# Kernel optimization log

Measured on AMD Instinct MI355X. Metric: run time of the kernel, lower is better.

## Reference

```python
import jax, jax.numpy as jnp
import numpy as np

B, N, D, E = 4, 1024, 1024, 8
TOP_N = 2
THRESHOLD = 0.2
EPS = 1e-9
CAP_FACTOR = 2.0
MIN_EXPERT_CAPACITY = 4
H = int(D * 4 * 2 / 3)  # GEGLU hidden = 2730


def setup_inputs() -> dict:
    key = jax.random.key(0)
    ks = jax.random.split(key, 8)
    u = lambda k, shape, fan: jax.random.uniform(k, shape, jnp.float32, -1.0, 1.0) * (fan ** -0.5)
    return {
        "x": jax.random.normal(ks[0], (B, N, D), jnp.float32),
        "route_probs": jax.random.uniform(ks[1], (TOP_N, B, N), jnp.float32),
        "gate_w": u(ks[2], (D, E), D),
        "w1": u(ks[3], (E, D, 2 * H), 2 * H),
        "b1": u(ks[4], (E, 2 * H), 2 * H),
        "mult_bias": jnp.ones((E, H), jnp.float32),
        "w2": u(ks[5], (E, H, D), D),
        "b2": u(ks[6], (E, D), D),
    }


def reference(x, route_probs, gate_w, w1, b1, mult_bias, w2, b2):
    b, n, d = x.shape
    e = gate_w.shape[1]
    cap = max(min(n, int(n * CAP_FACTOR / e)), MIN_EXPERT_CAPACITY)  # 256

    # ---- top-n gating ----
    logits = jnp.einsum('bnd,de->bne', x, gate_w)
    raw_gates = jax.nn.softmax(logits, axis=-1)
    gate_vals, gate_idx = jax.lax.top_k(raw_gates, TOP_N)          # [b,n,k]
    gate_vals = jnp.moveaxis(gate_vals, -1, 0)                      # [k,b,n]
    gate_idx = jnp.moveaxis(gate_idx, -1, 0)                        # [k,b,n]
    one_hot_idx = jax.nn.one_hot(gate_idx, e, dtype=x.dtype)        # [k,b,n,e]

    denom = jnp.clip(gate_vals.sum(axis=0, keepdims=True), EPS)
    gate_vals = gate_vals / denom

    # route to expert k>0 with prob min(1, gate/threshold); expert 0 always routed
    should_route = route_probs < (gate_vals / THRESHOLD)
    should_route = should_route.at[0].set(True)
    mask = one_hot_idx * should_route[..., None].astype(x.dtype)    # [k,b,n,e]

    # exclusive cumsum over sequence dim -> position within each expert
    mask_cumsum = jnp.cumsum(mask, axis=2) - mask                   # [k,b,n,e]

    positions, masks = [], []
    prev_count = jnp.zeros((b, 1, e), x.dtype)
    for k in range(TOP_N):  # small fixed loop over top-n
        pos_e = (mask_cumsum[k] + prev_count) * mask[k]             # [b,n,e]
        mk = mask[k] * (pos_e < float(cap)).astype(x.dtype)
        prev_count = prev_count + mk.sum(axis=1, keepdims=True)
        positions.append(pos_e.sum(axis=-1))                        # [b,n]
        masks.append(mk)
    positions = jnp.stack(positions)                                # [k,b,n]
    mask = jnp.stack(masks)                                         # [k,b,n,e]

    mask_flat = mask.sum(axis=-1)                                   # [k,b,n] in {0,1}
    gates = gate_vals * mask_flat
    pos_one_hot = jax.nn.one_hot(positions.astype(jnp.int32), cap, dtype=x.dtype)  # [k,b,n,c]

    # combine tensor [b,n,e,c]; dispatch is its boolean support
    combine = jnp.einsum('kbn,kbne,kbnc->bnec', gates * mask_flat, one_hot_idx, pos_one_hot)
    dispatch = (combine > 0).astype(x.dtype)

    # ---- dispatch tokens to experts ----
    xe = jnp.einsum('bnd,bnec->ebcd', x, dispatch)                  # [e,b,c,d]

    # ---- per-expert GEGLU FFN (grouped GEMM) ----
    h = jnp.einsum('ebcd,edf->ebcf', xe, w1) + b1[:, None, None, :]
    val, gate = jnp.split(h, 2, axis=-1)
    act = jax.nn.gelu(gate, approximate=False) * val * mult_bias[:, None, None, :]
    out_e = jnp.einsum('ebch,ehd->ebcd', act, w2) + b2[:, None, None, :]

    # ---- combine ----
    out = jnp.einsum('ebcd,bnec->bnd', out_e, combine)
    return out


if __name__ == '__main__':
    inp = setup_inputs()
    o = reference(**inp)
    print(o.shape, o.dtype)
```

## Files before the change

kernel.cpp:

```cpp
#include <hip/hip_runtime.h>
#include <hip/hip_bf16.h>
#include <math.h>

#define B_ 4
#define N_ 1024
#define D_ 1024
#define E_ 8
#define H_ 2730
#define H2_ 5460
#define CAP_ 256
#define NTOK 4096
#define NSLOT 8192
#define NKT1 16
#define NKT2 43
#define NFG 22

typedef __attribute__((ext_vector_type(8))) short short8;
typedef __attribute__((ext_vector_type(4))) float f32x4;

__device__ __forceinline__ unsigned short f2bf(float f) {
    __hip_bfloat16 h = __float2bfloat16(f);
    return *reinterpret_cast<unsigned short*>(&h);
}

#define GLL16(g, l)                                                          \
    __builtin_amdgcn_global_load_lds(                                        \
        (const __attribute__((address_space(1))) void*)(g),                  \
        (__attribute__((address_space(3))) void*)(l), 16, 0, 0)

#define VMCNT4() asm volatile("s_waitcnt vmcnt(4)" ::: "memory")
#define VMCNT3() asm volatile("s_waitcnt vmcnt(3)" ::: "memory")
#define VMCNT0() asm volatile("s_waitcnt vmcnt(0)" ::: "memory")
#define SBAR()   __builtin_amdgcn_s_barrier()
#define SCHEDB() __builtin_amdgcn_sched_barrier(0)


__global__ __launch_bounds__(256) void k_cvt1(const float* __restrict__ w1,
                                              unsigned short* __restrict__ w1p) {
    const int fg = blockIdx.x;
    const int kt = blockIdx.y;
    const int e  = blockIdx.z;
    const float* w1e = w1 + (size_t)e * D_ * H2_;
    unsigned short* dst = w1p + (((size_t)((e * NFG + fg) * NKT1 + kt)) << 14);
#pragma unroll
    for (int i = 0; i < 8; ++i) {
        const int o = i * 256 + threadIdx.x;
        const int l = o & 63, n16 = (o >> 6) & 15, k32 = o >> 10;
        const int f = fg * 128 + ((n16 & 7) << 4) + (l & 15);
        const int k = kt * 64 + (k32 << 5) + ((l >> 4) << 3);
        ushort4 r0 = {0, 0, 0, 0}, r1 = {0, 0, 0, 0};
        if (f < H_) {
            const float* s = w1e + (size_t)k * H2_ + (n16 >= 8 ? H_ : 0) + f;
            r0.x = f2bf(s[0]);
            r0.y = f2bf(s[(size_t)H2_]);
            r0.z = f2bf(s[(size_t)2 * H2_]);
            r0.w = f2bf(s[(size_t)3 * H2_]);
            r1.x = f2bf(s[(size_t)4 * H2_]);
            r1.y = f2bf(s[(size_t)5 * H2_]);
            r1.z = f2bf(s[(size_t)6 * H2_]);
            r1.w = f2bf(s[(size_t)7 * H2_]);
        }
        *reinterpret_cast<ushort4*>(dst + (size_t)o * 8) = r0;
        *reinterpret_cast<ushort4*>(dst + (size_t)o * 8 + 4) = r1;
    }
}

__global__ __launch_bounds__(256) void k_cvt2(const float* __restrict__ w2,
                                              unsigned short* __restrict__ w2p) {
    const int kt = blockIdx.x;
    const int nt = blockIdx.y;
    const int e  = blockIdx.z;
    const float* w2e = w2 + (size_t)e * H_ * D_;
    unsigned short* dst = w2p + (((size_t)((e * 8 + nt) * NKT2 + kt)) << 13);
#pragma unroll
    for (int i = 0; i < 4; ++i) {
        const int o = i * 256 + threadIdx.x;
        const int l = o & 63, n16 = (o >> 6) & 7, k32 = o >> 9;
        const int d = nt * 128 + (n16 << 4) + (l & 15);
        const int f = kt * 64 + (k32 << 5) + ((l >> 4) << 3);
        const float* s = w2e + (size_t)f * D_ + d;
        ushort4 r0, r1;
        r0.x = (f + 0 < H_) ? f2bf(s[0]) : 0;
        r0.y = (f + 1 < H_) ? f2bf(s[(size_t)D_]) : 0;
        r0.z = (f + 2 < H_) ? f2bf(s[(size_t)2 * D_]) : 0;
        r0.w = (f + 3 < H_) ? f2bf(s[(size_t)3 * D_]) : 0;
        r1.x = (f + 4 < H_) ? f2bf(s[(size_t)4 * D_]) : 0;
        r1.y = (f + 5 < H_) ? f2bf(s[(size_t)5 * D_]) : 0;
        r1.z = (f + 6 < H_) ? f2bf(s[(size_t)6 * D_]) : 0;
        r1.w = (f + 7 < H_) ? f2bf(s[(size_t)7 * D_]) : 0;
        *reinterpret_cast<ushort4*>(dst + (size_t)o * 8) = r0;
        *reinterpret_cast<ushort4*>(dst + (size_t)o * 8 + 4) = r1;
    }
}

__global__ __launch_bounds__(256) void k_gate(const float* __restrict__ x,
                                              const float* __restrict__ route,
                                              const float* __restrict__ gw,
                                              int* __restrict__ tokE,
                                              float* __restrict__ tokG,
                                              int* __restrict__ tokR) {
    const int wave = threadIdx.x >> 6, lane = threadIdx.x & 63;
    const int t = blockIdx.x * 4 + wave;
    float acc[E_];
#pragma unroll
    for (int e = 0; e < E_; ++e) acc[e] = 0.f;
    const float* xr = x + (size_t)t * D_;
    for (int d = lane; d < D_; d += 64) {
        float xv = xr[d];
        const float* g = gw + d * E_;
#pragma unroll
        for (int e = 0; e < E_; ++e) acc[e] = fmaf(xv, g[e], acc[e]);
    }
#pragma unroll
    for (int e = 0; e < E_; ++e) {
#pragma unroll
        for (int off = 32; off; off >>= 1) acc[e] += __shfl_xor(acc[e], off);
    }
    if (lane == 0) {
        float m = acc[0];
#pragma unroll
        for (int e = 1; e < E_; ++e) m = fmaxf(m, acc[e]);
        float p[E_]; float s = 0.f;
#pragma unroll
        for (int e = 0; e < E_; ++e) { p[e] = expf(acc[e] - m); s += p[e]; }
        int i0 = 0; float v0 = p[0];
#pragma unroll
        for (int e = 1; e < E_; ++e) if (p[e] > v0) { v0 = p[e]; i0 = e; }
        int i1 = (i0 == 0) ? 1 : 0; float v1 = p[i1];
#pragma unroll
        for (int e = 0; e < E_; ++e) if (e != i0 && p[e] > v1) { v1 = p[e]; i1 = e; }
        float p0 = v0 / s, p1 = v1 / s;
        float denom = fmaxf(p0 + p1, 1e-9f);
        float g0 = p0 / denom, g1 = p1 / denom;
        int r1 = route[NTOK + t] < (g1 / 0.2f);
        tokE[t] = i0; tokE[NTOK + t] = i1;
        tokG[t] = g0; tokG[NTOK + t] = g1;
        tokR[t] = r1;
    }
}

__global__ __launch_bounds__(256) void k_pos(const int* __restrict__ tokE,
                                             const float* __restrict__ tokG,
                                             const int* __restrict__ tokR,
                                             int* __restrict__ sot,
                                             int* __restrict__ tos) {
    const int e = blockIdx.x & 7, b = blockIdx.x >> 3;
    const int t = threadIdx.x;
    __shared__ int sc[256];
    const int base_bt = b * N_ + t * 4;
    int m0[4], m1[4];
    int c0 = 0, c1 = 0;
#pragma unroll
    for (int i = 0; i < 4; ++i) {
        int bt = base_bt + i;
        m0[i] = (tokE[bt] == e) ? 1 : 0;
        m1[i] = ((tokE[NTOK + bt] == e) && tokR[bt]) ? 1 : 0;
        c0 += m0[i]; c1 += m1[i];
    }
    int packed = c0 | (c1 << 16);
    sc[t] = packed;
    __syncthreads();
    for (int off = 1; off < 256; off <<= 1) {
        int v = (t >= off) ? sc[t - off] : 0;
        __syncthreads();
        sc[t] += v;
        __syncthreads();
    }
    int incl = sc[t];
    int total = sc[255];
    int excl = incl - packed;
    int base0 = excl & 0xffff;
    int base1 = excl >> 16;
    int kept0 = min(total & 0xffff, CAP_);
#pragma unroll
    for (int i = 0; i < 4; ++i) {
        int bt = base_bt + i;
        if (m0[i]) {
            int pos = base0++;
            if (pos < CAP_ && tokG[bt] > 0.f) {
                int s = ((e * B_ + b) << 8) + pos;
                sot[bt] = s;
                tos[s] = bt;
            }
        }
        if (m1[i]) {
            int pos = (base1++) + kept0;
            if (pos < CAP_ && tokG[NTOK + bt] > 0.f) {
                int s = ((e * B_ + b) << 8) + pos;
                sot[NTOK + bt] = s;
                tos[s] = bt;
            }
        }
    }
}

__global__ __launch_bounds__(256) void k_disp(const float* __restrict__ x,
                                              const int* __restrict__ tos,
                                              unsigned short* __restrict__ xeP) {
    const int t = threadIdx.x;
    const int s = blockIdx.x * 2 + (t >> 7);
    const int q = t & 127;
    const int bt = tos[s];
    const int kt = q >> 3, k32 = (q >> 2) & 1, kq = q & 3;
    const int lane = (kq << 4) | (s & 15);
    const int m16 = (s >> 4) & 15;
    const int sgrp = s >> 8;
    unsigned short* dst = xeP + (((size_t)(sgrp * NKT1 + kt)) << 14) + (k32 << 13) + (m16 << 9) + lane * 8;
    ushort4 r0 = {0, 0, 0, 0}, r1 = {0, 0, 0, 0};
    if (bt >= 0) {
        const float4 v0 = *reinterpret_cast<const float4*>(x + ((size_t)bt << 10) + q * 8);
        const float4 v1 = *reinterpret_cast<const float4*>(x + ((size_t)bt << 10) + q * 8 + 4);
        r0.x = f2bf(v0.x); r0.y = f2bf(v0.y); r0.z = f2bf(v0.z); r0.w = f2bf(v0.w);
        r1.x = f2bf(v1.x); r1.y = f2bf(v1.y); r1.z = f2bf(v1.z); r1.w = f2bf(v1.w);
    }
    *reinterpret_cast<ushort4*>(dst) = r0;
    *reinterpret_cast<ushort4*>(dst + 4) = r1;
}

__global__ __launch_bounds__(512) void k_ffn1(const unsigned short* __restrict__ xeP,
                                              const unsigned short* __restrict__ w1p,
                                              const float* __restrict__ b1,
                                              const float* __restrict__ mbias,
                                              unsigned short* __restrict__ actP) {
    const int wg = blockIdx.x;
    const int e = wg & 7;
    const int rem = wg >> 3;
    const int fg = rem >> 2;
    const int rt = rem & 3;
    const int sgrp = e * 4 + rt;

    __shared__ unsigned short Ab[2][16384];
    __shared__ unsigned short Bb[2][16384];

    const int tid = threadIdx.x, lane = tid & 63, w = tid >> 6;
    const int wm = w >> 2, wn = w & 3;
    const int lane8 = lane * 8;
    const int woff = w * 1024;
    const int am0 = wm * 8, bn0 = wn * 2;

    const unsigned short* abase = xeP + ((size_t)(sgrp * NKT1) << 14);
    const unsigned short* bbase = w1p + ((size_t)((e * NFG + fg) * NKT1) << 14);

    f32x4 acc[8][4];
#pragma unroll
    for (int i = 0; i < 8; ++i)
#pragma unroll
        for (int j = 0; j < 4; ++j) acc[i][j] = (f32x4)(0.f);

#define LDA1(ks, m16) (*reinterpret_cast<const short8*>(&Ab[cur][(((ks) << 4) + (m16)) * 512 + lane8]))
#define LDB1(ks, n16) (*reinterpret_cast<const short8*>(&Bb[cur][(((ks) << 4) + (n16)) * 512 + lane8]))

    {
#pragma unroll
        for (int hq = 0; hq < 2; ++hq) {
            const int off = hq * 8192 + woff;
            GLL16(abase + off + lane8, (char*)&Ab[0][off]);
            GLL16(abase + off + 512 + lane8, (char*)&Ab[0][off + 512]);
            GLL16(bbase + off + lane8, (char*)&Bb[0][off]);
            GLL16(bbase + off + 512 + lane8, (char*)&Bb[0][off + 512]);
        }
    }

    for (int kt = 0; kt < NKT1; ++kt) {
        const int cur = kt & 1, nx = cur ^ 1;
        const bool pf = (kt + 1 < NKT1);
        const unsigned short* asn = abase + ((size_t)(kt + 1) << 14);
        const unsigned short* bsn = bbase + ((size_t)(kt + 1) << 14);
        short8 af[4], bf[4];

        SCHEDB(); VMCNT4(); SBAR(); SCHEDB();

        if (pf) {
            GLL16(asn + woff + lane8, (char*)&Ab[nx][woff]);
            GLL16(asn + woff + 512 + lane8, (char*)&Ab[nx][woff + 512]);
        }
        bf[0] = LDB1(0, bn0); bf[1] = LDB1(0, bn0 + 1);
        bf[2] = LDB1(0, bn0 + 8); bf[3] = LDB1(0, bn0 + 9);
        af[0] = LDA1(0, am0 + 0); af[1] = LDA1(0, am0 + 1);
        af[2] = LDA1(0, am0 + 2); af[3] = LDA1(0, am0 + 3);
        __builtin_amdgcn_s_setprio(1);
#pragma unroll
        for (int mi = 0; mi < 4; ++mi)
#pragma unroll
            for (int n = 0; n < 4; ++n)
                acc[mi][n] = __builtin_amdgcn_mfma_f32_16x16x32_bf16(af[mi], bf[n], acc[mi][n], 0, 0, 0);
        __builtin_amdgcn_s_setprio(0);

        if (pf) {
            GLL16(bsn + woff + lane8, (char*)&Bb[nx][woff]);
            GLL16(bsn + woff + 512 + lane8, (char*)&Bb[nx][woff + 512]);
        }
        af[0] = LDA1(0, am0 + 4); af[1] = LDA1(0, am0 + 5);
        af[2] = LDA1(0, am0 + 6); af[3] = LDA1(0, am0 + 7);
        __builtin_amdgcn_s_setprio(1);
#pragma unroll
        for (int mi = 0; mi < 4; ++mi)
#pragma unroll
            for (int n = 0; n < 4; ++n)
                acc[4 + mi][n] = __builtin_amdgcn_mfma_f32_16x16x32_bf16(af[mi], bf[n], acc[4 + mi][n], 0, 0, 0);
        __builtin_amdgcn_s_setprio(0);

        SCHEDB();
        if (pf) { VMCNT4(); } else { VMCNT0(); }
        SBAR(); SCHEDB();

        if (pf) {
            const int off = 8192 + woff;
            GLL16(asn + off + lane8, (char*)&Ab[nx][off]);
            GLL16(asn + off + 512 + lane8, (char*)&Ab[nx][off + 512]);
        }
        bf[0] = LDB1(1, bn0); bf[1] = LDB1(1, bn0 + 1);
        bf[2] = LDB1(1, bn0 + 8); bf[3] = LDB1(1, bn0 + 9);
        af[0] = LDA1(1, am0 + 0); af[1] = LDA1(1, am0 + 1);
        af[2] = LDA1(1, am0 + 2); af[3] = LDA1(1, am0 + 3);
        __builtin_amdgcn_s_setprio(1);
#pragma unroll
        for (int mi = 0; mi < 4; ++mi)
#pragma unroll
            for (int n = 0; n < 4; ++n)
                acc[mi][n] = __builtin_amdgcn_mfma_f32_16x16x32_bf16(af[mi], bf[n], acc[mi][n], 0, 0, 0);
        __builtin_amdgcn_s_setprio(0);

        if (pf) {
            const int off = 8192 + woff;
            GLL16(bsn + off + lane8, (char*)&Bb[nx][off]);
            GLL16(bsn + off + 512 + lane8, (char*)&Bb[nx][off + 512]);
        }
        af[0] = LDA1(1, am0 + 4); af[1] = LDA1(1, am0 + 5);
        af[2] = LDA1(1, am0 + 6); af[3] = LDA1(1, am0 + 7);
        __builtin_amdgcn_s_setprio(1);
#pragma unroll
        for (int mi = 0; mi < 4; ++mi)
#pragma unroll
            for (int n = 0; n < 4; ++n)
                acc[4 + mi][n] = __builtin_amdgcn_mfma_f32_16x16x32_bf16(af[mi], bf[n], acc[4 + mi][n], 0, 0, 0);
        __builtin_amdgcn_s_setprio(0);
    }
#undef LDA1
#undef LDB1

    const float* b1e = b1 + (size_t)e * H2_;
    const float* mbe = mbias + (size_t)e * H_;
    const int colL = lane & 15, rq4 = (lane >> 4) * 4;
#pragma unroll
    for (int mi = 0; mi < 8; ++mi) {
        const int Rl = wm * 128 + mi * 16 + rq4;
#pragma unroll
        for (int vi = 0; vi < 2; ++vi) {
            const int f = fg * 128 + wn * 32 + vi * 16 + colL;
            if (f >= NKT2 * 64) continue;
            const bool real = f < H_;
            const float bv = real ? b1e[f] : 0.f;
            const float bg = real ? b1e[H_ + f] : 0.f;
            const float mv = real ? mbe[f] : 0.f;
            const int ktf = f >> 6, k32f = (f >> 5) & 1;
            const int lhi = ((f >> 3) & 3) << 4;
            const int bb = f & 7;
            const size_t cbase = ((size_t)(sgrp * NKT2 + ktf) << 14) + (k32f << 13);
#pragma unroll
            for (int j = 0; j < 4; ++j) {
                const int R = Rl + j;
                float a = 0.f;
                if (real) {
                    const float val = acc[mi][vi][j] + bv;
                    const float gt  = acc[mi][2 + vi][j] + bg;
                    a = 0.5f * gt * (1.f + erff(gt * 0.70710678118654752f)) * val * mv;
                }
                actP[cbase + ((R >> 4) << 9) + (size_t)((lhi | (R & 15)) * 8 + bb)] = f2bf(a);
            }
        }
    }
}

__global__ __launch_bounds__(512) void k_ffn2(const unsigned short* __restrict__ actP,
                                              const unsigned short* __restrict__ w2p,
                                              const float* __restrict__ b2,
                                              float* __restrict__ oute) {
    const int wg = blockIdx.x;
    const int e = wg & 7;
    const int rem = wg >> 3;
    const int nt = rem >> 2;
    const int mt = rem & 3;
    const int sgrp = e * 4 + mt;

    __shared__ unsigned short Ab[2][16384];
    __shared__ unsigned short Bb[2][8192];

    const int tid = threadIdx.x, lane = tid & 63, w = tid >> 6;
    const int wm = w >> 2, wn = w & 3;
    const int lane8 = lane * 8;
    const int woff = w * 1024;
    const int woffb = w * 512;
    const int am0 = wm * 8, bn0 = wn * 2;

    const unsigned short* abase = actP + ((size_t)(sgrp * NKT2) << 14);
    const unsigned short* bbase = w2p + ((size_t)((e * 8 + nt) * NKT2) << 13);

    f32x4 acc[8][2];
#pragma unroll
    for (int i = 0; i < 8; ++i)
#pragma unroll
        for (int j = 0; j < 2; ++j) acc[i][j] = (f32x4)(0.f);

#define LDA2(ks, m16) (*reinterpret_cast<const short8*>(&Ab[cur][(((ks) << 4) + (m16)) * 512 + lane8]))
#define LDB2(ks, n16) (*reinterpret_cast<const short8*>(&Bb[cur][((ks) * 8 + (n16)) * 512 + lane8]))

    {
#pragma unroll
        for (int hq = 0; hq < 2; ++hq) {
            const int off = hq * 8192 + woff;
            GLL16(abase + off + lane8, (char*)&Ab[0][off]);
            GLL16(abase + off + 512 + lane8, (char*)&Ab[0][off + 512]);
            const int boff = hq * 4096 + woffb;
            GLL16(bbase + boff + lane8, (char*)&Bb[0][boff]);
        }
    }

    for (int kt = 0; kt < NKT2; ++kt) {
        const int cur = kt & 1, nx = cur ^ 1;
        const bool pf = (kt + 1 < NKT2);
        const unsigned short* asn = abase + ((size_t)(kt + 1) << 14);
        const unsigned short* bsn = bbase + ((size_t)(kt + 1) << 13);
        short8 af[4], bf[2];

        SCHEDB(); VMCNT3(); SBAR(); SCHEDB();

        if (pf) {
            GLL16(asn + woff + lane8, (char*)&Ab[nx][woff]);
            GLL16(asn + woff + 512 + lane8, (char*)&Ab[nx][woff + 512]);
        }
        bf[0] = LDB2(0, bn0); bf[1] = LDB2(0, bn0 + 1);
        af[0] = LDA2(0, am0 + 0); af[1] = LDA2(0, am0 + 1);
        af[2] = LDA2(0, am0 + 2); af[3] = LDA2(0, am0 + 3);
        __builtin_amdgcn_s_setprio(1);
#pragma unroll
        for (int mi = 0; mi < 4; ++mi)
#pragma unroll
            for (int n = 0; n < 2; ++n)
                acc[mi][n] = __builtin_amdgcn_mfma_f32_16x16x32_bf16(af[mi], bf[n], acc[mi][n], 0, 0, 0);
        __builtin_amdgcn_s_setprio(0);

        if (pf) {
            GLL16(bsn + woffb + lane8, (char*)&Bb[nx][woffb]);
        }
        af[0] = LDA2(0, am0 + 4); af[1] = LDA2(0, am0 + 5);
        af[2] = LDA2(0, am0 + 6); af[3] = LDA2(0, am0 + 7);
        __builtin_amdgcn_s_setprio(1);
#pragma unroll
        for (int mi = 0; mi < 4; ++mi)
#pragma unroll
            for (int n = 0; n < 2; ++n)
                acc[4 + mi][n] = __builtin_amdgcn_mfma_f32_16x16x32_bf16(af[mi], bf[n], acc[4 + mi][n], 0, 0, 0);
        __builtin_amdgcn_s_setprio(0);

        SCHEDB();
        if (pf) { VMCNT3(); } else { VMCNT0(); }
        SBAR(); SCHEDB();

        if (pf) {
            const int off = 8192 + woff;
            GLL16(asn + off + lane8, (char*)&Ab[nx][off]);
            GLL16(asn + off + 512 + lane8, (char*)&Ab[nx][off + 512]);
        }
        bf[0] = LDB2(1, bn0); bf[1] = LDB2(1, bn0 + 1);
        af[0] = LDA2(1, am0 + 0); af[1] = LDA2(1, am0 + 1);
        af[2] = LDA2(1, am0 + 2); af[3] = LDA2(1, am0 + 3);
        __builtin_amdgcn_s_setprio(1);
#pragma unroll
        for (int mi = 0; mi < 4; ++mi)
#pragma unroll
            for (int n = 0; n < 2; ++n)
                acc[mi][n] = __builtin_amdgcn_mfma_f32_16x16x32_bf16(af[mi], bf[n], acc[mi][n], 0, 0, 0);
        __builtin_amdgcn_s_setprio(0);

        if (pf) {
            const int boff = 4096 + woffb;
            GLL16(bsn + boff + lane8, (char*)&Bb[nx][boff]);
        }
        af[0] = LDA2(1, am0 + 4); af[1] = LDA2(1, am0 + 5);
        af[2] = LDA2(1, am0 + 6); af[3] = LDA2(1, am0 + 7);
        __builtin_amdgcn_s_setprio(1);
#pragma unroll
        for (int mi = 0; mi < 4; ++mi)
#pragma unroll
            for (int n = 0; n < 2; ++n)
                acc[4 + mi][n] = __builtin_amdgcn_mfma_f32_16x16x32_bf16(af[mi], bf[n], acc[4 + mi][n], 0, 0, 0);
        __builtin_amdgcn_s_setprio(0);
    }
#undef LDA2
#undef LDB2

    const float* b2e = b2 + (size_t)e * D_;
    const int colL = lane & 15, rq4 = (lane >> 4) * 4;
#pragma unroll
    for (int mi = 0; mi < 8; ++mi) {
#pragma unroll
        for (int vi = 0; vi < 2; ++vi) {
            const int d = nt * 128 + wn * 32 + vi * 16 + colL;
            const float bb2 = b2e[d];
#pragma unroll
            for (int j = 0; j < 4; ++j) {
                const int R = mt * 256 + wm * 128 + mi * 16 + rq4 + j;
                oute[((size_t)(e * 1024 + R) << 10) + d] = acc[mi][vi][j] + bb2;
            }
        }
    }
}

__global__ __launch_bounds__(256) void k_comb(const float* __restrict__ oute,
                                              const int* __restrict__ sot,
                                              const float* __restrict__ tokG,
                                              float* __restrict__ out) {
    const int bt = blockIdx.x;
    const int t = threadIdx.x;
    const int s0 = sot[bt], s1 = sot[NTOK + bt];
    const float g0 = tokG[bt], g1 = tokG[NTOK + bt];
    float r0 = 0.f, r1 = 0.f, r2 = 0.f, r3 = 0.f;
    if (s0 >= 0) {
        const float4 v = *reinterpret_cast<const float4*>(oute + ((size_t)s0 << 10) + t * 4);
        r0 += g0 * v.x; r1 += g0 * v.y; r2 += g0 * v.z; r3 += g0 * v.w;
    }
    if (s1 >= 0) {
        const float4 v = *reinterpret_cast<const float4*>(oute + ((size_t)s1 << 10) + t * 4);
        r0 += g1 * v.x; r1 += g1 * v.y; r2 += g1 * v.z; r3 += g1 * v.w;
    }
    float4 o; o.x = r0; o.y = r1; o.z = r2; o.w = r3;
    *reinterpret_cast<float4*>(out + ((size_t)bt << 10) + t * 4) = o;
}

extern "C" void kernel_launch(void* const* d_in, const int* in_sizes, int n_in,
                              void* d_out, int out_size, void* d_ws, size_t ws_size,
                              hipStream_t stream) {
    const float* x     = (const float*)d_in[0];
    const float* route = (const float*)d_in[1];
    const float* gw    = (const float*)d_in[2];
    const float* w1    = (const float*)d_in[3];
    const float* b1    = (const float*)d_in[4];
    const float* mb    = (const float*)d_in[5];
    const float* w2    = (const float*)d_in[6];
    const float* b2    = (const float*)d_in[7];
    float* out = (float*)d_out;

    char* ws = (char*)d_ws;
    int*   tokE = (int*)(ws + 0);
    float* tokG = (float*)(ws + 32768);
    int*   tokR = (int*)(ws + 65536);
    int*   sot  = (int*)(ws + 81920);
    int*   tos  = (int*)(ws + 114688);
    unsigned short* xeP  = (unsigned short*)(ws + 147456);
    unsigned short* actP = (unsigned short*)(ws + 16924672);
    unsigned short* w1p  = (unsigned short*)(ws + 62013440);
    unsigned short* w2p  = (unsigned short*)(ws + 62013440);
    float* oute = (float*)(ws + 107102208);

    hipMemsetAsync(sot, 0xFF, 65536, stream);

    k_cvt1<<<dim3(NFG, NKT1, 8), 256, 0, stream>>>(w1, w1p);
    k_gate<<<NTOK / 4, 256, 0, stream>>>(x, route, gw, tokE, tokG, tokR);
    k_pos<<<E_ * B_, 256, 0, stream>>>(tokE, tokG, tokR, sot, tos);
    k_disp<<<NSLOT / 2, 256, 0, stream>>>(x, tos, xeP);
    k_ffn1<<<704, 512, 0, stream>>>(xeP, w1p, b1, mb, actP);
    k_cvt2<<<dim3(NKT2, 8, 8), 256, 0, stream>>>(w2, w2p);
    k_ffn2<<<256, 512, 0, stream>>>(actP, w2p, b2, oute);
    k_comb<<<NTOK, 256, 0, stream>>>(oute, sot, tokG, out);
}
```

Measured before the change: 370.4 us.

## Unroll GEMM k-loops by two with static LDS buffers and store expert outputs as bf16

Both grouped GEMM kernels now unroll their k-tile loop by two and alternate between separately named LDS buffers. Buffer indices are compile-time constants, which removes runtime buffer indexing and may let the compiler schedule LDS reads and MFMAs more freely. Separately, the second FFN writes its per-expert outputs in bf16 instead of fp32, and the combine kernel reads and widens them, halving the intermediate write and read traffic. This costs some precision on the expert outputs before the gated combine.

```diff
diff --git a/kernel.cpp b/kernel.cpp
--- a/kernel.cpp
+++ b/kernel.cpp
@@ -22,6 +22,10 @@
     __hip_bfloat16 h = __float2bfloat16(f);
     return *reinterpret_cast<unsigned short*>(&h);
 }
+__device__ __forceinline__ float bf2f(unsigned short u) {
+    unsigned x = ((unsigned)u) << 16;
+    union { unsigned u; float f; } c; c.u = x; return c.f;
+}
 
 #define GLL16(g, l)                                                          \
     __builtin_amdgcn_global_load_lds(                                        \
@@ -33,6 +37,7 @@
 #define VMCNT0() asm volatile("s_waitcnt vmcnt(0)" ::: "memory")
 #define SBAR()   __builtin_amdgcn_s_barrier()
 #define SCHEDB() __builtin_amdgcn_sched_barrier(0)
+#define MFMA16(a, b, c) __builtin_amdgcn_mfma_f32_16x16x32_bf16((a), (b), (c), 0, 0, 0)
 
 
 __global__ __launch_bounds__(256) void k_cvt1(const float* __restrict__ w1,
@@ -217,6 +222,80 @@
     *reinterpret_cast<ushort4*>(dst + 4) = r1;
 }
 
+#define LDF(BUF, idx) (*reinterpret_cast<const short8*>(&BUF[(idx) * 512 + lane8]))
+
+#define FFN1_MM03(AF0, AF1, AF2, AF3)                                         \
+    do {                                                                      \
+        acc[0][0]=MFMA16(AF0,bf0,acc[0][0]); acc[0][1]=MFMA16(AF0,bf1,acc[0][1]); \
+        acc[0][2]=MFMA16(AF0,bf2,acc[0][2]); acc[0][3]=MFMA16(AF0,bf3,acc[0][3]); \
+        acc[1][0]=MFMA16(AF1,bf0,acc[1][0]); acc[1][1]=MFMA16(AF1,bf1,acc[1][1]); \
+        acc[1][2]=MFMA16(AF1,bf2,acc[1][2]); acc[1][3]=MFMA16(AF1,bf3,acc[1][3]); \
+        acc[2][0]=MFMA16(AF2,bf0,acc[2][0]); acc[2][1]=MFMA16(AF2,bf1,acc[2][1]); \
+        acc[2][2]=MFMA16(AF2,bf2,acc[2][2]); acc[2][3]=MFMA16(AF2,bf3,acc[2][3]); \
+        acc[3][0]=MFMA16(AF3,bf0,acc[3][0]); acc[3][1]=MFMA16(AF3,bf1,acc[3][1]); \
+        acc[3][2]=MFMA16(AF3,bf2,acc[3][2]); acc[3][3]=MFMA16(AF3,bf3,acc[3][3]); \
+    } while (0)
+#define FFN1_MM47(AF0, AF1, AF2, AF3)                                         \
+    do {                                                                      \
+        acc[4][0]=MFMA16(AF0,bf0,acc[4][0]); acc[4][1]=MFMA16(AF0,bf1,acc[4][1]); \
+        acc[4][2]=MFMA16(AF0,bf2,acc[4][2]); acc[4][3]=MFMA16(AF0,bf3,acc[4][3]); \
+        acc[5][0]=MFMA16(AF1,bf0,acc[5][0]); acc[5][1]=MFMA16(AF1,bf1,acc[5][1]); \
+        acc[5][2]=MFMA16(AF1,bf2,acc[5][2]); acc[5][3]=MFMA16(AF1,bf3,acc[5][3]); \
+        acc[6][0]=MFMA16(AF2,bf0,acc[6][0]); acc[6][1]=MFMA16(AF2,bf1,acc[6][1]); \
+        acc[6][2]=MFMA16(AF2,bf2,acc[6][2]); acc[6][3]=MFMA16(AF2,bf3,acc[6][3]); \
+        acc[7][0]=MFMA16(AF3,bf0,acc[7][0]); acc[7][1]=MFMA16(AF3,bf1,acc[7][1]); \
+        acc[7][2]=MFMA16(AF3,bf2,acc[7][2]); acc[7][3]=MFMA16(AF3,bf3,acc[7][3]); \
+    } while (0)
+
+#define FFN1_KT(ARD, BRD, AWR, BWR, KTN, PF)                                  \
+    do {                                                                      \
+        const unsigned short* asn = abase + ((size_t)(KTN) << 14);            \
+        const unsigned short* bsn = bbase + ((size_t)(KTN) << 14);            \
+        short8 af0, af1, af2, af3, bf0, bf1, bf2, bf3;                        \
+        SCHEDB(); VMCNT4(); SBAR(); SCHEDB();                                 \
+        if (PF) {                                                             \
+            GLL16(asn + woff + lane8, (char*)&AWR[woff]);                     \
+            GLL16(asn + woff + 512 + lane8, (char*)&AWR[woff + 512]);         \
+        }                                                                     \
+        bf0 = LDF(BRD, bn0); bf1 = LDF(BRD, bn0 + 1);                         \
+        bf2 = LDF(BRD, bn0 + 8); bf3 = LDF(BRD, bn0 + 9);                     \
+        af0 = LDF(ARD, am0 + 0); af1 = LDF(ARD, am0 + 1);                     \
+        af2 = LDF(ARD, am0 + 2); af3 = LDF(ARD, am0 + 3);                     \
+        __builtin_amdgcn_s_setprio(1);                                        \
+        FFN1_MM03(af0, af1, af2, af3);                                        \
+        __builtin_amdgcn_s_setprio(0);                                        \
+        if (PF) {                                                             \
+            GLL16(bsn + woff + lane8, (char*)&BWR[woff]);                     \
+            GLL16(bsn + woff + 512 + lane8, (char*)&BWR[woff + 512]);         \
+        }                                                                     \
+        af0 = LDF(ARD, am0 + 4); af1 = LDF(ARD, am0 + 5);                     \
+        af2 = LDF(ARD, am0 + 6); af3 = LDF(ARD, am0 + 7);                     \
+        __builtin_amdgcn_s_setprio(1);                                        \
+        FFN1_MM47(af0, af1, af2, af3);                                        \
+        __builtin_amdgcn_s_setprio(0);                                        \
+        SCHEDB(); if (PF) { VMCNT4(); } else { VMCNT0(); } SBAR(); SCHEDB();  \
+        if (PF) {                                                             \
+            GLL16(asn + 8192 + woff + lane8, (char*)&AWR[8192 + woff]);       \
+            GLL16(asn + 8192 + woff + 512 + lane8, (char*)&AWR[8192 + woff + 512]); \
+        }                                                                     \
+        bf0 = LDF(BRD, 16 + bn0); bf1 = LDF(BRD, 16 + bn0 + 1);               \
+        bf2 = LDF(BRD, 16 + bn0 + 8); bf3 = LDF(BRD, 16 + bn0 + 9);           \
+        af0 = LDF(ARD, 16 + am0 + 0); af1 = LDF(ARD, 16 + am0 + 1);           \
+        af2 = LDF(ARD, 16 + am0 + 2); af3 = LDF(ARD, 16 + am0 + 3);           \
+        __builtin_amdgcn_s_setprio(1);                                        \
+        FFN1_MM03(af0, af1, af2, af3);                                        \
+        __builtin_amdgcn_s_setprio(0);                                        \
+        if (PF) {                                                             \
+            GLL16(bsn + 8192 + woff + lane8, (char*)&BWR[8192 + woff]);       \
+            GLL16(bsn + 8192 + woff + 512 + lane8, (char*)&BWR[8192 + woff + 512]); \
+        }                                                                     \
+        af0 = LDF(ARD, 16 + am0 + 4); af1 = LDF(ARD, 16 + am0 + 5);           \
+        af2 = LDF(ARD, 16 + am0 + 6); af3 = LDF(ARD, 16 + am0 + 7);           \
+        __builtin_amdgcn_s_setprio(1);                                        \
+        FFN1_MM47(af0, af1, af2, af3);                                        \
+        __builtin_amdgcn_s_setprio(0);                                        \
+    } while (0)
+
 __global__ __launch_bounds__(512) void k_ffn1(const unsigned short* __restrict__ xeP,
                                               const unsigned short* __restrict__ w1p,
                                               const float* __restrict__ b1,
@@ -229,8 +308,10 @@
     const int rt = rem & 3;
     const int sgrp = e * 4 + rt;
 
-    __shared__ unsigned short Ab[2][16384];
-    __shared__ unsigned short Bb[2][16384];
+    __shared__ unsigned short Ab0[16384];
+    __shared__ unsigned short Bb0[16384];
+    __shared__ unsigned short Ab1[16384];
+    __shared__ unsigned short Bb1[16384];
 
     const int tid = threadIdx.x, lane = tid & 63, w = tid >> 6;
     const int wm = w >> 2, wn = w & 3;
@@ -247,97 +328,19 @@
 #pragma unroll
         for (int j = 0; j < 4; ++j) acc[i][j] = (f32x4)(0.f);
 
-#define LDA1(ks, m16) (*reinterpret_cast<const short8*>(&Ab[cur][(((ks) << 4) + (m16)) * 512 + lane8]))
-#define LDB1(ks, n16) (*reinterpret_cast<const short8*>(&Bb[cur][(((ks) << 4) + (n16)) * 512 + lane8]))
-
-    {
-#pragma unroll
-        for (int hq = 0; hq < 2; ++hq) {
-            const int off = hq * 8192 + woff;
-            GLL16(abase + off + lane8, (char*)&Ab[0][off]);
-            GLL16(abase + off + 512 + lane8, (char*)&Ab[0][off + 512]);
-            GLL16(bbase + off + lane8, (char*)&Bb[0][off]);
-            GLL16(bbase + off + 512 + lane8, (char*)&Bb[0][off + 512]);
-        }
-    }
-
-    for (int kt = 0; kt < NKT1; ++kt) {
-        const int cur = kt & 1, nx = cur ^ 1;
-        const bool pf = (kt + 1 < NKT1);
-        const unsigned short* asn = abase + ((size_t)(kt + 1) << 14);
-        const unsigned short* bsn = bbase + ((size_t)(kt + 1) << 14);
-        short8 af[4], bf[4];
-
-        SCHEDB(); VMCNT4(); SBAR(); SCHEDB();
-
-        if (pf) {
-            GLL16(asn + woff + lane8, (char*)&Ab[nx][woff]);
-            GLL16(asn + woff + 512 + lane8, (char*)&Ab[nx][woff + 512]);
-        }
-        bf[0] = LDB1(0, bn0); bf[1] = LDB1(0, bn0 + 1);
-        bf[2] = LDB1(0, bn0 + 8); bf[3] = LDB1(0, bn0 + 9);
-        af[0] = LDA1(0, am0 + 0); af[1] = LDA1(0, am0 + 1);
-        af[2] = LDA1(0, am0 + 2); af[3] = LDA1(0, am0 + 3);
-        __builtin_amdgcn_s_setprio(1);
-#pragma unroll
-        for (int mi = 0; mi < 4; ++mi)
-#pragma unroll
-            for (int n = 0; n < 4; ++n)
-                acc[mi][n] = __builtin_amdgcn_mfma_f32_16x16x32_bf16(af[mi], bf[n], acc[mi][n], 0, 0, 0);
-        __builtin_amdgcn_s_setprio(0);
-
-        if (pf) {
-            GLL16(bsn + woff + lane8, (char*)&Bb[nx][woff]);
-            GLL16(bsn + woff + 512 + lane8, (char*)&Bb[nx][woff + 512]);
-        }
-        af[0] = LDA1(0, am0 + 4); af[1] = LDA1(0, am0 + 5);
-        af[2] = LDA1(0, am0 + 6); af[3] = LDA1(0, am0 + 7);
-        __builtin_amdgcn_s_setprio(1);
-#pragma unroll
-        for (int mi = 0; mi < 4; ++mi)
-#pragma unroll
-            for (int n = 0; n < 4; ++n)
-                acc[4 + mi][n] = __builtin_amdgcn_mfma_f32_16x16x32_bf16(af[mi], bf[n], acc[4 + mi][n], 0, 0, 0);
-        __builtin_amdgcn_s_setprio(0);
-
-        SCHEDB();
-        if (pf) { VMCNT4(); } else { VMCNT0(); }
-        SBAR(); SCHEDB();
-
-        if (pf) {
-            const int off = 8192 + woff;
-            GLL16(asn + off + lane8, (char*)&Ab[nx][off]);
-            GLL16(asn + off + 512 + lane8, (char*)&Ab[nx][off + 512]);
-        }
-        bf[0] = LDB1(1, bn0); bf[1] = LDB1(1, bn0 + 1);
-        bf[2] = LDB1(1, bn0 + 8); bf[3] = LDB1(1, bn0 + 9);
-        af[0] = LDA1(1, am0 + 0); af[1] = LDA1(1, am0 + 1);
-        af[2] = LDA1(1, am0 + 2); af[3] = LDA1(1, am0 + 3);
-        __builtin_amdgcn_s_setprio(1);
-#pragma unroll
-        for (int mi = 0; mi < 4; ++mi)
-#pragma unroll
-            for (int n = 0; n < 4; ++n)
-                acc[mi][n] = __builtin_amdgcn_mfma_f32_16x16x32_bf16(af[mi], bf[n], acc[mi][n], 0, 0, 0);
-        __builtin_amdgcn_s_setprio(0);
-
-        if (pf) {
-            const int off = 8192 + woff;
-            GLL16(bsn + off + lane8, (char*)&Bb[nx][off]);
-            GLL16(bsn + off + 512 + lane8, (char*)&Bb[nx][off + 512]);
-        }
-        af[0] = LDA1(1, am0 + 4); af[1] = LDA1(1, am0 + 5);
-        af[2] = LDA1(1, am0 + 6); af[3] = LDA1(1, am0 + 7);
-        __builtin_amdgcn_s_setprio(1);
-#pragma unroll
-        for (int mi = 0; mi < 4; ++mi)
-#pragma unroll
-            for (int n = 0; n < 4; ++n)
-                acc[4 + mi][n] = __builtin_amdgcn_mfma_f32_16x16x32_bf16(af[mi], bf[n], acc[4 + mi][n], 0, 0, 0);
-        __builtin_amdgcn_s_setprio(0);
-    }
-#undef LDA1
-#undef LDB1
+    GLL16(abase + woff + lane8, (char*)&Ab0[woff]);
+    GLL16(abase + woff + 512 + lane8, (char*)&Ab0[woff + 512]);
+    GLL16(bbase + woff + lane8, (char*)&Bb0[woff]);
+    GLL16(bbase + woff + 512 + lane8, (char*)&Bb0[woff + 512]);
+    GLL16(abase + 8192 + woff + lane8, (char*)&Ab0[8192 + woff]);
+    GLL16(abase + 8192 + woff + 512 + lane8, (char*)&Ab0[8192 + woff + 512]);
+    GLL16(bbase + 8192 + woff + lane8, (char*)&Bb0[8192 + woff]);
+    GLL16(bbase + 8192 + woff + 512 + lane8, (char*)&Bb0[8192 + woff + 512]);
+
+    for (int kt = 0; kt < NKT1; kt += 2) {
+        FFN1_KT(Ab0, Bb0, Ab1, Bb1, kt + 1, 1);
+        FFN1_KT(Ab1, Bb1, Ab0, Bb0, kt + 2, (kt + 2) < NKT1);
+    }
 
     const float* b1e = b1 + (size_t)e * H2_;
     const float* mbe = mbias + (size_t)e * H_;
@@ -372,10 +375,66 @@
     }
 }
 
+#define FFN2_MM03(AF0, AF1, AF2, AF3)                                         \
+    do {                                                                      \
+        acc[0][0]=MFMA16(AF0,bf0,acc[0][0]); acc[0][1]=MFMA16(AF0,bf1,acc[0][1]); \
+        acc[1][0]=MFMA16(AF1,bf0,acc[1][0]); acc[1][1]=MFMA16(AF1,bf1,acc[1][1]); \
+        acc[2][0]=MFMA16(AF2,bf0,acc[2][0]); acc[2][1]=MFMA16(AF2,bf1,acc[2][1]); \
+        acc[3][0]=MFMA16(AF3,bf0,acc[3][0]); acc[3][1]=MFMA16(AF3,bf1,acc[3][1]); \
+    } while (0)
+#define FFN2_MM47(AF0, AF1, AF2, AF3)                                         \
+    do {                                                                      \
+        acc[4][0]=MFMA16(AF0,bf0,acc[4][0]); acc[4][1]=MFMA16(AF0,bf1,acc[4][1]); \
+        acc[5][0]=MFMA16(AF1,bf0,acc[5][0]); acc[5][1]=MFMA16(AF1,bf1,acc[5][1]); \
+        acc[6][0]=MFMA16(AF2,bf0,acc[6][0]); acc[6][1]=MFMA16(AF2,bf1,acc[6][1]); \
+        acc[7][0]=MFMA16(AF3,bf0,acc[7][0]); acc[7][1]=MFMA16(AF3,bf1,acc[7][1]); \
+    } while (0)
+
+#define FFN2_KT(ARD, BRD, AWR, BWR, KTN, PF)                                  \
+    do {                                                                      \
+        const unsigned short* asn = abase + ((size_t)(KTN) << 14);            \
+        const unsigned short* bsn = bbase + ((size_t)(KTN) << 13);            \
+        short8 af0, af1, af2, af3, bf0, bf1;                                  \
+        SCHEDB(); VMCNT3(); SBAR(); SCHEDB();                                 \
+        if (PF) {                                                             \
+            GLL16(asn + woff + lane8, (char*)&AWR[woff]);                     \
+            GLL16(asn + woff + 512 + lane8, (char*)&AWR[woff + 512]);         \
+        }                                                                     \
+        bf0 = LDF(BRD, bn0); bf1 = LDF(BRD, bn0 + 1);                         \
+        af0 = LDF(ARD, am0 + 0); af1 = LDF(ARD, am0 + 1);                     \
+        af2 = LDF(ARD, am0 + 2); af3 = LDF(ARD, am0 + 3);                     \
+        __builtin_amdgcn_s_setprio(1);                                        \
+        FFN2_MM03(af0, af1, af2, af3);                                        \
+        __builtin_amdgcn_s_setprio(0);                                        \
+        if (PF) { GLL16(bsn + woffb + lane8, (char*)&BWR[woffb]); }           \
+        af0 = LDF(ARD, am0 + 4); af1 = LDF(ARD, am0 + 5);                     \
+        af2 = LDF(ARD, am0 + 6); af3 = LDF(ARD, am0 + 7);                     \
+        __builtin_amdgcn_s_setprio(1);                                        \
+        FFN2_MM47(af0, af1, af2, af3);                                        \
+        __builtin_amdgcn_s_setprio(0);                                        \
+        SCHEDB(); if (PF) { VMCNT3(); } else { VMCNT0(); } SBAR(); SCHEDB();  \
+        if (PF) {                                                             \
+            GLL16(asn + 8192 + woff + lane8, (char*)&AWR[8192 + woff]);       \
+            GLL16(asn + 8192 + woff + 512 + lane8, (char*)&AWR[8192 + woff + 512]); \
+        }                                                                     \
+        bf0 = LDF(BRD, 8 + bn0); bf1 = LDF(BRD, 8 + bn0 + 1);                 \
+        af0 = LDF(ARD, 16 + am0 + 0); af1 = LDF(ARD, 16 + am0 + 1);           \
+        af2 = LDF(ARD, 16 + am0 + 2); af3 = LDF(ARD, 16 + am0 + 3);           \
+        __builtin_amdgcn_s_setprio(1);                                        \
+        FFN2_MM03(af0, af1, af2, af3);                                        \
+        __builtin_amdgcn_s_setprio(0);                                        \
+        if (PF) { GLL16(bsn + 4096 + woffb + lane8, (char*)&BWR[4096 + woffb]); } \
+        af0 = LDF(ARD, 16 + am0 + 4); af1 = LDF(ARD, 16 + am0 + 5);           \
+        af2 = LDF(ARD, 16 + am0 + 6); af3 = LDF(ARD, 16 + am0 + 7);           \
+        __builtin_amdgcn_s_setprio(1);                                        \
+        FFN2_MM47(af0, af1, af2, af3);                                        \
+        __builtin_amdgcn_s_setprio(0);                                        \
+    } while (0)
+
 __global__ __launch_bounds__(512) void k_ffn2(const unsigned short* __restrict__ actP,
                                               const unsigned short* __restrict__ w2p,
                                               const float* __restrict__ b2,
-                                              float* __restrict__ oute) {
+                                              unsigned short* __restrict__ oute) {
     const int wg = blockIdx.x;
     const int e = wg & 7;
     const int rem = wg >> 3;
@@ -383,8 +442,10 @@
     const int mt = rem & 3;
     const int sgrp = e * 4 + mt;
 
-    __shared__ unsigned short Ab[2][16384];
-    __shared__ unsigned short Bb[2][8192];
+    __shared__ unsigned short Ab0[16384];
+    __shared__ unsigned short Bb0[8192];
+    __shared__ unsigned short Ab1[16384];
+    __shared__ unsigned short Bb1[8192];
 
     const int tid = threadIdx.x, lane = tid & 63, w = tid >> 6;
     const int wm = w >> 2, wn = w & 3;
@@ -402,93 +463,18 @@
 #pragma unroll
         for (int j = 0; j < 2; ++j) acc[i][j] = (f32x4)(0.f);
 
-#define LDA2(ks, m16) (*reinterpret_cast<const short8*>(&Ab[cur][(((ks) << 4) + (m16)) * 512 + lane8]))
-#define LDB2(ks, n16) (*reinterpret_cast<const short8*>(&Bb[cur][((ks) * 8 + (n16)) * 512 + lane8]))
-
-    {
-#pragma unroll
-        for (int hq = 0; hq < 2; ++hq) {
-            const int off = hq * 8192 + woff;
-            GLL16(abase + off + lane8, (char*)&Ab[0][off]);
-            GLL16(abase + off + 512 + lane8, (char*)&Ab[0][off + 512]);
-            const int boff = hq * 4096 + woffb;
-            GLL16(bbase + boff + lane8, (char*)&Bb[0][boff]);
-        }
-    }
-
-    for (int kt = 0; kt < NKT2; ++kt) {
-        const int cur = kt & 1, nx = cur ^ 1;
-        const bool pf = (kt + 1 < NKT2);
-        const unsigned short* asn = abase + ((size_t)(kt + 1) << 14);
-        const unsigned short* bsn = bbase + ((size_t)(kt + 1) << 13);
-        short8 af[4], bf[2];
-
-        SCHEDB(); VMCNT3(); SBAR(); SCHEDB();
-
-        if (pf) {
-            GLL16(asn + woff + lane8, (char*)&Ab[nx][woff]);
-            GLL16(asn + woff + 512 + lane8, (char*)&Ab[nx][woff + 512]);
-        }
-        bf[0] = LDB2(0, bn0); bf[1] = LDB2(0, bn0 + 1);
-        af[0] = LDA2(0, am0 + 0); af[1] = LDA2(0, am0 + 1);
-        af[2] = LDA2(0, am0 + 2); af[3] = LDA2(0, am0 + 3);
-        __builtin_amdgcn_s_setprio(1);
-#pragma unroll
-        for (int mi = 0; mi < 4; ++mi)
-#pragma unroll
-            for (int n = 0; n < 2; ++n)
-                acc[mi][n] = __builtin_amdgcn_mfma_f32_16x16x32_bf16(af[mi], bf[n], acc[mi][n], 0, 0, 0);
-        __builtin_amdgcn_s_setprio(0);
-
-        if (pf) {
-            GLL16(bsn + woffb + lane8, (char*)&Bb[nx][woffb]);
-        }
-        af[0] = LDA2(0, am0 + 4); af[1] = LDA2(0, am0 + 5);
-        af[2] = LDA2(0, am0 + 6); af[3] = LDA2(0, am0 + 7);
-        __builtin_amdgcn_s_setprio(1);
-#pragma unroll
-        for (int mi = 0; mi < 4; ++mi)
-#pragma unroll
-            for (int n = 0; n < 2; ++n)
-                acc[4 + mi][n] = __builtin_amdgcn_mfma_f32_16x16x32_bf16(af[mi], bf[n], acc[4 + mi][n], 0, 0, 0);
-        __builtin_amdgcn_s_setprio(0);
-
-        SCHEDB();
-        if (pf) { VMCNT3(); } else { VMCNT0(); }
-        SBAR(); SCHEDB();
-
-        if (pf) {
-            const int off = 8192 + woff;
-            GLL16(asn + off + lane8, (char*)&Ab[nx][off]);
-            GLL16(asn + off + 512 + lane8, (char*)&Ab[nx][off + 512]);
-        }
-        bf[0] = LDB2(1, bn0); bf[1] = LDB2(1, bn0 + 1);
-        af[0] = LDA2(1, am0 + 0); af[1] = LDA2(1, am0 + 1);
-        af[2] = LDA2(1, am0 + 2); af[3] = LDA2(1, am0 + 3);
-        __builtin_amdgcn_s_setprio(1);
-#pragma unroll
-        for (int mi = 0; mi < 4; ++mi)
-#pragma unroll
-            for (int n = 0; n < 2; ++n)
-                acc[mi][n] = __builtin_amdgcn_mfma_f32_16x16x32_bf16(af[mi], bf[n], acc[mi][n], 0, 0, 0);
-        __builtin_amdgcn_s_setprio(0);
-
-        if (pf) {
-            const int boff = 4096 + woffb;
-            GLL16(bsn + boff + lane8, (char*)&Bb[nx][boff]);
-        }
-        af[0] = LDA2(1, am0 + 4); af[1] = LDA2(1, am0 + 5);
-        af[2] = LDA2(1, am0 + 6); af[3] = LDA2(1, am0 + 7);
-        __builtin_amdgcn_s_setprio(1);
-#pragma unroll
-        for (int mi = 0; mi < 4; ++mi)
-#pragma unroll
-            for (int n = 0; n < 2; ++n)
-                acc[4 + mi][n] = __builtin_amdgcn_mfma_f32_16x16x32_bf16(af[mi], bf[n], acc[4 + mi][n], 0, 0, 0);
-        __builtin_amdgcn_s_setprio(0);
-    }
-#undef LDA2
-#undef LDB2
+    GLL16(abase + woff + lane8, (char*)&Ab0[woff]);
+    GLL16(abase + woff + 512 + lane8, (char*)&Ab0[woff + 512]);
+    GLL16(bbase + woffb + lane8, (char*)&Bb0[woffb]);
+    GLL16(abase + 8192 + woff + lane8, (char*)&Ab0[8192 + woff]);
+    GLL16(abase + 8192 + woff + 512 + lane8, (char*)&Ab0[8192 + woff + 512]);
+    GLL16(bbase + 4096 + woffb + lane8, (char*)&Bb0[4096 + woffb]);
+
+    for (int kt = 0; kt < NKT2 - 1; kt += 2) {
+        FFN2_KT(Ab0, Bb0, Ab1, Bb1, kt + 1, 1);
+        FFN2_KT(Ab1, Bb1, Ab0, Bb0, kt + 2, (kt + 2) < NKT2);
+    }
+    FFN2_KT(Ab0, Bb0, Ab1, Bb1, NKT2, 0);
 
     const float* b2e = b2 + (size_t)e * D_;
     const int colL = lane & 15, rq4 = (lane >> 4) * 4;
@@ -501,13 +487,13 @@
 #pragma unroll
             for (int j = 0; j < 4; ++j) {
                 const int R = mt * 256 + wm * 128 + mi * 16 + rq4 + j;
-                oute[((size_t)(e * 1024 + R) << 10) + d] = acc[mi][vi][j] + bb2;
+                oute[((size_t)(e * 1024 + R) << 10) + d] = f2bf(acc[mi][vi][j] + bb2);
             }
         }
     }
 }
 
-__global__ __launch_bounds__(256) void k_comb(const float* __restrict__ oute,
+__global__ __launch_bounds__(256) void k_comb(const unsigned short* __restrict__ oute,
                                               const int* __restrict__ sot,
                                               const float* __restrict__ tokG,
                                               float* __restrict__ out) {
@@ -517,12 +503,12 @@
     const float g0 = tokG[bt], g1 = tokG[NTOK + bt];
     float r0 = 0.f, r1 = 0.f, r2 = 0.f, r3 = 0.f;
     if (s0 >= 0) {
-        const float4 v = *reinterpret_cast<const float4*>(oute + ((size_t)s0 << 10) + t * 4);
-        r0 += g0 * v.x; r1 += g0 * v.y; r2 += g0 * v.z; r3 += g0 * v.w;
+        const ushort4 v = *reinterpret_cast<const ushort4*>(oute + ((size_t)s0 << 10) + t * 4);
+        r0 += g0 * bf2f(v.x); r1 += g0 * bf2f(v.y); r2 += g0 * bf2f(v.z); r3 += g0 * bf2f(v.w);
     }
     if (s1 >= 0) {
-        const float4 v = *reinterpret_cast<const float4*>(oute + ((size_t)s1 << 10) + t * 4);
-        r0 += g1 * v.x; r1 += g1 * v.y; r2 += g1 * v.z; r3 += g1 * v.w;
+        const ushort4 v = *reinterpret_cast<const ushort4*>(oute + ((size_t)s1 << 10) + t * 4);
+        r0 += g1 * bf2f(v.x); r1 += g1 * bf2f(v.y); r2 += g1 * bf2f(v.z); r3 += g1 * bf2f(v.w);
     }
     float4 o; o.x = r0; o.y = r1; o.z = r2; o.w = r3;
     *reinterpret_cast<float4*>(out + ((size_t)bt << 10) + t * 4) = o;
@@ -551,7 +537,7 @@
     unsigned short* actP = (unsigned short*)(ws + 16924672);
     unsigned short* w1p  = (unsigned short*)(ws + 62013440);
     unsigned short* w2p  = (unsigned short*)(ws + 62013440);
-    float* oute = (float*)(ws + 107102208);
+    unsigned short* oute = (unsigned short*)(ws + 107102208);
 
     hipMemsetAsync(sot, 0xFF, 65536, stream);
 
```

Result: faster. 325.6 us (-12.1%).
